# Kernel optimization log

Measured on AMD Instinct MI355X. Metric: run time of the kernel, lower is better.

## Reference

```python
import jax, jax.numpy as jnp
import numpy as np

BN_EPS = 1e-5
K = 9  # 3x3 kernel positions


def conv2d(x, w, b, pad, dil=1):
    out = jax.lax.conv_general_dilated(
        x, w, window_strides=(1, 1), padding=((pad, pad), (pad, pad)),
        rhs_dilation=(dil, dil), dimension_numbers=('NCHW', 'OIHW', 'NCHW'))
    return out + b[None, :, None, None]


def bn_relu(x, g, be, mu, var):
    inv = jax.lax.rsqrt(var + BN_EPS)
    return jax.nn.relu((x - mu[None, :, None, None]) * (g * inv)[None, :, None, None] + be[None, :, None, None])


def deform_conv(x, w_om, b_om, w, b):
    # DCNv2-style modulated deformable 3x3 conv, stride 1, pad 1, dg=1.
    B, C, H, W = x.shape
    om = conv2d(x, w_om, b_om, pad=1)               # [B, 27, H, W]
    o1, o2, m = jnp.split(om, 3, axis=1)            # dy, dx, mask logits: [B,9,H,W]
    mask = jax.nn.sigmoid(m)
    ky, kx = jnp.meshgrid(jnp.arange(3), jnp.arange(3), indexing='ij')
    ky = (ky.reshape(-1) - 1).astype(x.dtype)       # kernel offsets in {-1,0,1}
    kx = (kx.reshape(-1) - 1).astype(x.dtype)
    py = jnp.arange(H, dtype=x.dtype)[None, None, :, None] + ky[None, :, None, None] + o1  # [B,9,H,W]
    px = jnp.arange(W, dtype=x.dtype)[None, None, None, :] + kx[None, :, None, None] + o2

    y0 = jnp.floor(py); x0 = jnp.floor(px)
    wy1 = py - y0; wx1 = px - x0
    y0i = y0.astype(jnp.int32); x0i = x0.astype(jnp.int32)
    x_flat = x.reshape(B, C, H * W)

    def corner(yi, xi, wgt):
        valid = ((yi >= 0) & (yi < H) & (xi >= 0) & (xi < W)).astype(x.dtype)
        idx = jnp.clip(yi, 0, H - 1) * W + jnp.clip(xi, 0, W - 1)      # [B,9,H,W]
        g = jax.vmap(lambda xf, i: xf[:, i])(x_flat, idx.reshape(B, -1))
        g = g.reshape(B, C, K, H, W)
        return g * (wgt * valid)[:, None]

    cols = (corner(y0i,     x0i,     (1 - wy1) * (1 - wx1))
            + corner(y0i,     x0i + 1, (1 - wy1) * wx1)
            + corner(y0i + 1, x0i,     wy1 * (1 - wx1))
            + corner(y0i + 1, x0i + 1, wy1 * wx1))                       # [B,C,9,H,W]
    cols = cols * mask[:, None]
    out = jnp.einsum('bckhw,ock->bohw', cols, w.reshape(w.shape[0], C, K))
    return out + b[None, :, None, None]


def setup_inputs() -> dict:
    key = jax.random.key(0)
    ks = jax.random.split(key, 24)
    B, C, H, W = 2, 64, 256, 256
    d = {}
    d['x'] = jax.random.normal(ks[0], (B, C, H, W), jnp.float32)
    d['w_om'] = jax.random.normal(ks[1], (27, C, 3, 3), jnp.float32) * 0.01
    d['b_om'] = jax.random.normal(ks[2], (27,), jnp.float32) * 0.01
    d['w_dcn'] = jax.random.normal(ks[3], (C, C, 3, 3), jnp.float32) * 0.05
    d['b_dcn'] = jax.random.normal(ks[4], (C,), jnp.float32) * 0.05
    for i, pfx in enumerate(['bn1', 'bn2', 'bn3']):
        d[pfx + '_g'] = jax.random.uniform(ks[5 + 4 * i], (C,), jnp.float32, 0.5, 1.5)
        d[pfx + '_b'] = jax.random.normal(ks[6 + 4 * i], (C,), jnp.float32) * 0.05
        d[pfx + '_m'] = jax.random.normal(ks[7 + 4 * i], (C,), jnp.float32) * 0.05
        d[pfx + '_v'] = jax.random.uniform(ks[8 + 4 * i], (C,), jnp.float32, 0.5, 1.5)
    d['w_h'] = jax.random.normal(ks[17], (C, C, 3, 3), jnp.float32) * 0.05
    d['b_h'] = jax.random.normal(ks[18], (C,), jnp.float32) * 0.05
    d['w_w'] = jax.random.normal(ks[19], (C, C, 3, 3), jnp.float32) * 0.05
    d['b_w'] = jax.random.normal(ks[20], (C,), jnp.float32) * 0.05
    d['w3'] = jax.random.normal(ks[21], (1, C, 3, 3), jnp.float32) * 0.05
    d['b3'] = jax.random.normal(ks[22], (1,), jnp.float32) * 0.05
    return d


def reference(x, w_om, b_om, w_dcn, b_dcn,
              bn1_g, bn1_b, bn1_m, bn1_v,
              w_h, b_h, bn2_g, bn2_b, bn2_m, bn2_v,
              w_w, b_w, bn3_g, bn3_b, bn3_m, bn3_v,
              w3, b3):
    h = deform_conv(x, w_om, b_om, w_dcn, b_dcn)
    h = bn_relu(h, bn1_g, bn1_b, bn1_m, bn1_v)
    h = conv2d(h, w_h, b_h, pad=2, dil=2)
    h = bn_relu(h, bn2_g, bn2_b, bn2_m, bn2_v)
    h = conv2d(h, w_w, b_w, pad=2, dil=2)
    h = bn_relu(h, bn3_g, bn3_b, bn3_m, bn3_v)
    h = conv2d(h, w3, b3, pad=1)
    return jnp.clip(jax.nn.sigmoid(h), 1e-4, 1.0 - 1e-4)
```

## Files before the change

### kernel.cpp

```cpp
#include <hip/hip_runtime.h>
#include <math.h>

#define HH 256
#define WW 256
#define HW (HH*WW)
#define NPX (2*HW)

typedef __attribute__((ext_vector_type(8))) short bf16x8;
typedef __attribute__((ext_vector_type(8))) _Float16 f16x8;
typedef __attribute__((ext_vector_type(2))) _Float16 f16x2;
typedef __attribute__((ext_vector_type(4))) float f32x4;

__device__ __forceinline__ float bf2f(short h) {
    union { unsigned u; float f; } v; v.u = ((unsigned)(unsigned short)h) << 16; return v.f;
}
__device__ __forceinline__ short f2bf(float f) {
    union { float f; unsigned u; } v; v.f = f;
    unsigned r = v.u + 0x7fffu + ((v.u >> 16) & 1u);
    return (short)(r >> 16);
}
__device__ __forceinline__ short f2hs(float f) {
    _Float16 h = (_Float16)f;
    union { _Float16 h; short s; } v; v.h = h; return v.s;
}

__global__ __launch_bounds__(256) void k_x2cl(const float* __restrict__ x,
        short* __restrict__ xcl,
        const float* __restrict__ w_om, const float* __restrict__ w_dcn,
        const float* __restrict__ w_h,  const float* __restrict__ w_w,
        const float* __restrict__ w3,
        short* __restrict__ wt_om, short* __restrict__ wt_dcn,
        short* __restrict__ wt_h,  short* __restrict__ wt_w,
        float* __restrict__ w3t) {
    __shared__ short tile[256 * 66];
    const int xx = threadIdx.x;
    const int row = blockIdx.x;
    const int b = row >> 8, y = row & 255;
    for (int c = 0; c < 64; ++c)
        tile[xx * 66 + c] = f2hs(x[((b * 64 + c) << 16) + (y << 8) + xx]);
    int i = blockIdx.x * 256 + threadIdx.x;
    if (i < 64 * 576) {
        int o = i / 576, k = i - o * 576, t = k >> 6, c = k & 63;
        int kb = k >> 3, j = k & 7;
        int src = (o * 64 + c) * 9 + t;
        int dst = (kb * 64 + o) * 8 + j;
        wt_dcn[dst] = f2hs(w_dcn[src]);
        wt_h[dst]   = f2bf(w_h[src]);
        wt_w[dst]   = f2bf(w_w[src]);
        if (o < 32) wt_om[(kb * 32 + o) * 8 + j] = (o < 27) ? f2hs(w_om[src]) : (short)0;
        if (o == 0) w3t[k] = w3[c * 9 + t];
    }
    __syncthreads();
    short* op = xcl + ((row << 8) + xx) * 64;
#pragma unroll
    for (int j = 0; j < 8; ++j) {
        bf16x8 v;
#pragma unroll
        for (int e = 0; e < 8; ++e) v[e] = tile[xx * 66 + j * 8 + e];
        *(bf16x8*)(op + j * 8) = v;
    }
}

#define XPS 72

__global__ __launch_bounds__(256) __attribute__((amdgpu_waves_per_eu(2, 4)))
void k_dcn_mfma(const short* __restrict__ xcl,
        const short* __restrict__ wom, const float* __restrict__ b_om,
        const short* __restrict__ wt,
        const float* __restrict__ bias,
        const float* __restrict__ gg, const float* __restrict__ be,
        const float* __restrict__ mu, const float* __restrict__ var,
        short* __restrict__ out_cl) {
    __shared__ short xt[256 * XPS];
    __shared__ _Float16 om_lds[64 * 28];
    const int lane = threadIdx.x & 63, wave = threadIdx.x >> 6;
    const int quad = lane >> 4, l16 = lane & 15;
    const int band = blockIdx.x & 7, idx = blockIdx.x >> 3;
    const int tr = band * 8 + (idx >> 5), tc = idx & 31;
    const int b = tr >> 5;
    const int ty0 = (tr & 31) * 8, tx0 = tc * 8;
    const int base = b << 16;
    const int hy0 = ty0 - 4, hx0 = tx0 - 4;
    {
        const int p = threadIdx.x;
        const int sy = min(max(hy0 + (p >> 4), 0), 255);
        const int sx = min(max(hx0 + (p & 15), 0), 255);
        const short* src = xcl + (size_t)((base + sy * 256 + sx) * 64);
        short* dst = &xt[p * XPS];
#pragma unroll
        for (int j = 0; j < 8; ++j)
            *(bf16x8*)(dst + j * 8) = *(const bf16x8*)(src + j * 8);
    }
    __syncthreads();

    const int lp = wave * 16 + l16;
    const int pyy = lp >> 3, pxx = lp & 7;
    const int y = ty0 + pyy, x = tx0 + pxx;

    {
        f32x4 oacc[2];
        oacc[0] = (f32x4){0,0,0,0}; oacc[1] = (f32x4){0,0,0,0};
        auto loadOB = [&](int s, f16x8* Bv) {
            const int kb = s * 4 + quad;
#pragma unroll
            for (int g = 0; g < 2; ++g)
                Bv[g] = *(const f16x8*)(wom + (kb * 32 + g * 16 + l16) * 8);
        };
        f16x8 OB[2][2];
        loadOB(0, OB[0]);
#pragma unroll
        for (int s = 0; s < 18; ++s) {
            if (s < 17) loadOB(s + 1, OB[(s + 1) & 1]);
            const int t = s >> 1, c0 = (s & 1) * 32;
            const int dy = t / 3 - 1, dx = t % 3 - 1;
            f16x8 av = *(const f16x8*)&xt[((pyy + 4 + dy) * 16 + (pxx + 4 + dx)) * XPS + c0 + quad * 8];
            bool ok = ((unsigned)(y + dy) < 256u) && ((unsigned)(x + dx) < 256u);
            if (!ok) { f16x8 z = {0,0,0,0,0,0,0,0}; av = z; }
#pragma unroll
            for (int g = 0; g < 2; ++g)
                oacc[g] = __builtin_amdgcn_mfma_f32_16x16x32_f16(av, OB[s & 1][g], oacc[g], 0, 0, 0);
        }
#pragma unroll
        for (int g = 0; g < 2; ++g) {
            int o = g * 16 + l16;
            if (o < 27) {
                float bo = b_om[o];
#pragma unroll
                for (int r = 0; r < 4; ++r) {
                    float v = oacc[g][r] + bo;
                    if (o >= 18) v = 1.f / (1.f + expf(-v));
                    om_lds[(wave * 16 + quad * 4 + r) * 28 + o] = (_Float16)v;
                }
            }
        }
    }
    __syncthreads();

    f32x4 acc[4];
#pragma unroll
    for (int i = 0; i < 4; ++i) acc[i] = (f32x4){0,0,0,0};

    float omr[27];
#pragma unroll
    for (int j = 0; j < 27; ++j) omr[j] = (float)om_lds[lp * 28 + j];

#pragma unroll
    for (int t = 0; t < 9; ++t) {
        const int ky = t / 3 - 1, kx = t % 3 - 1;
        float o1 = omr[t], o2 = omr[9 + t], m = omr[18 + t];
        float py = (float)(y + ky) + o1;
        float px = (float)(x + kx) + o2;
        float y0f = floorf(py), x0f = floorf(px);
        float wy1 = py - y0f, wx1 = px - x0f;
        int y0 = (int)y0f, xi0 = (int)x0f, y1 = y0 + 1, xi1 = xi0 + 1;
        float w00 = (1.f - wy1) * (1.f - wx1) * m;
        float w01 = (1.f - wy1) * wx1 * m;
        float w10 = wy1 * (1.f - wx1) * m;
        float w11 = wy1 * wx1 * m;
        if (!((unsigned)y0  < 256u)) { w00 = 0.f; w01 = 0.f; }
        if (!((unsigned)y1  < 256u)) { w10 = 0.f; w11 = 0.f; }
        if (!((unsigned)xi0 < 256u)) { w00 = 0.f; w10 = 0.f; }
        if (!((unsigned)xi1 < 256u)) { w01 = 0.f; w11 = 0.f; }
        int cy0 = min(max(y0, 0), 255), cy1 = min(max(y1, 0), 255);
        int cx0 = min(max(xi0, 0), 255), cx1 = min(max(xi1, 0), 255);
        int iy0 = cy0 - hy0, iy1 = cy1 - hy0;
        int ix0 = cx0 - hx0, ix1 = cx1 - hx0;
        bool inh = ((unsigned)iy0 < 16u) && ((unsigned)iy1 < 16u)
                && ((unsigned)ix0 < 16u) && ((unsigned)ix1 < 16u);

        f16x8 C[2][4];
        if (__all(inh)) {
            const int p00 = (iy0 * 16 + ix0) * XPS, p01 = (iy0 * 16 + ix1) * XPS;
            const int p10 = (iy1 * 16 + ix0) * XPS, p11 = (iy1 * 16 + ix1) * XPS;
#pragma unroll
            for (int h = 0; h < 2; ++h) {
                const int cb = h * 32 + quad * 8;
                C[h][0] = *(const f16x8*)&xt[p00 + cb];
                C[h][1] = *(const f16x8*)&xt[p01 + cb];
                C[h][2] = *(const f16x8*)&xt[p10 + cb];
                C[h][3] = *(const f16x8*)&xt[p11 + cb];
            }
        } else {
            const int i00 = (base + cy0 * 256 + cx0) * 64;
            const int i01 = (base + cy0 * 256 + cx1) * 64;
            const int i10 = (base + cy1 * 256 + cx0) * 64;
            const int i11 = (base + cy1 * 256 + cx1) * 64;
#pragma unroll
            for (int h = 0; h < 2; ++h) {
                const int cb = h * 32 + quad * 8;
                C[h][0] = *(const f16x8*)(xcl + i00 + cb);
                C[h][1] = *(const f16x8*)(xcl + i01 + cb);
                C[h][2] = *(const f16x8*)(xcl + i10 + cb);
                C[h][3] = *(const f16x8*)(xcl + i11 + cb);
            }
        }
        const _Float16 h00 = (_Float16)w00, h01 = (_Float16)w01;
        const _Float16 h10 = (_Float16)w10, h11 = (_Float16)w11;
        const f16x2 W00 = {h00, h00}, W01 = {h01, h01};
        const f16x2 W10 = {h10, h10}, W11 = {h11, h11};
#pragma unroll
        for (int h = 0; h < 2; ++h) {
            const f16x2* c0 = (const f16x2*)&C[h][0];
            const f16x2* c1 = (const f16x2*)&C[h][1];
            const f16x2* c2 = (const f16x2*)&C[h][2];
            const f16x2* c3 = (const f16x2*)&C[h][3];
            f16x8 av;
            f16x2* avp = (f16x2*)&av;
#pragma unroll
            for (int d = 0; d < 4; ++d) {
                f16x2 s = c0[d] * W00;
                s = __builtin_elementwise_fma(c1[d], W01, s);
                s = __builtin_elementwise_fma(c2[d], W10, s);
                s = __builtin_elementwise_fma(c3[d], W11, s);
                avp[d] = s;
            }
            const int kb = t * 8 + h * 4 + quad;
#pragma unroll
            for (int g = 0; g < 4; ++g) {
                f16x8 bv = *(const f16x8*)(wt + (kb * 64 + g * 16 + l16) * 8);
                acc[g] = __builtin_amdgcn_mfma_f32_16x16x32_f16(av, bv, acc[g], 0, 0, 0);
            }
        }
    }
#pragma unroll
    for (int g = 0; g < 4; ++g) {
        int o = g * 16 + l16;
        float sc = gg[o] * rsqrtf(var[o] + 1e-5f);
        float off = (bias[o] - mu[o]) * sc + be[o];
#pragma unroll
        for (int r = 0; r < 4; ++r) {
            int mm = quad * 4 + r;
            int pix = base + ((ty0 + wave * 2 + (mm >> 3)) << 8) + tx0 + (mm & 7);
            float v = acc[g][r] * sc + off;
            out_cl[(size_t)pix * 64 + o] = f2bf(fmaxf(v, 0.f));
        }
    }
}

__global__ __launch_bounds__(512) __attribute__((amdgpu_waves_per_eu(2, 4)))
void k_conv_mfma(const short* __restrict__ in_cl,
        const short* __restrict__ wt, const float* __restrict__ bias,
        const float* __restrict__ gg, const float* __restrict__ be,
        const float* __restrict__ mu, const float* __restrict__ var,
        short* __restrict__ out_cl) {
    __shared__ short xt[400 * XPS];
    const int lane = threadIdx.x & 63, wave = threadIdx.x >> 6;
    const int quad = lane >> 4, l16 = lane & 15;
    const int tIdx = (blockIdx.x & 7) * 64 + (blockIdx.x >> 3);
    const int tr = tIdx >> 4, tc = tIdx & 15;
    const int b = tr >> 4;
    const int ty0 = (tr & 15) * 16, tx0 = tc * 16;
    const int base = b << 16;
    if (threadIdx.x < 400) {
        const int p = threadIdx.x;
        const int sy = ty0 - 2 + p / 20, sx = tx0 - 2 + p % 20;
        short* dst = &xt[p * XPS];
        if (((unsigned)sy < 256u) && ((unsigned)sx < 256u)) {
            const short* src = in_cl + (size_t)((base + sy * 256 + sx) * 64);
#pragma unroll
            for (int j = 0; j < 8; ++j)
                *(bf16x8*)(dst + j * 8) = *(const bf16x8*)(src + j * 8);
        } else {
            bf16x8 z = {0,0,0,0,0,0,0,0};
#pragma unroll
            for (int j = 0; j < 8; ++j) *(bf16x8*)(dst + j * 8) = z;
        }
    }
    __syncthreads();
    const int ly = wave * 2;
    f32x4 acc[2][4];
#pragma unroll
    for (int h = 0; h < 2; ++h)
#pragma unroll
        for (int g = 0; g < 4; ++g) acc[h][g] = (f32x4){0,0,0,0};

    auto loadB = [&](int s, bf16x8* Bv) {
        const int kb = s * 4 + quad;
#pragma unroll
        for (int g = 0; g < 4; ++g)
            Bv[g] = *(const bf16x8*)(wt + (kb * 64 + g * 16 + l16) * 8);
    };
    bf16x8 B[3][4];
    loadB(0, B[0]);
    loadB(1, B[1]);
#pragma unroll
    for (int s = 0; s < 18; ++s) {
        if (s + 2 < 18) loadB(s + 2, B[(s + 2) % 3]);
        const int t = s >> 1, c0 = (s & 1) * 32;
        const int dy = (t / 3 - 1) * 2, dx = (t % 3 - 1) * 2;
        const int cidx = c0 + quad * 8;
        bf16x8 a0 = *(const bf16x8*)&xt[((ly + 2 + dy) * 20 + (l16 + 2 + dx)) * XPS + cidx];
        bf16x8 a1 = *(const bf16x8*)&xt[((ly + 3 + dy) * 20 + (l16 + 2 + dx)) * XPS + cidx];
#pragma unroll
        for (int g = 0; g < 4; ++g) {
            acc[0][g] = __builtin_amdgcn_mfma_f32_16x16x32_bf16(a0, B[s % 3][g], acc[0][g], 0, 0, 0);
            acc[1][g] = __builtin_amdgcn_mfma_f32_16x16x32_bf16(a1, B[s % 3][g], acc[1][g], 0, 0, 0);
        }
    }
#pragma unroll
    for (int h = 0; h < 2; ++h)
#pragma unroll
    for (int g = 0; g < 4; ++g) {
        int o = g * 16 + l16;
        float sc = gg[o] * rsqrtf(var[o] + 1e-5f);
        float off = (bias[o] - mu[o]) * sc + be[o];
#pragma unroll
        for (int r = 0; r < 4; ++r) {
            int pix = base + ((ty0 + ly + h) << 8) + tx0 + quad * 4 + r;
            float v = acc[h][g][r] * sc + off;
            out_cl[(size_t)pix * 64 + o] = f2bf(fmaxf(v, 0.f));
        }
    }
}

__global__ __launch_bounds__(256) void k_final(const short* __restrict__ h_cl,
        const float* __restrict__ w3t, const float* __restrict__ b3,
        float* __restrict__ out) {
    __shared__ short xt[324 * XPS];
    const int tIdx = (blockIdx.x & 7) * 64 + (blockIdx.x >> 3);
    const int tr = tIdx >> 4, tc = tIdx & 15;
    const int b = tr >> 4;
    const int ty0 = (tr & 15) * 16, tx0 = tc * 16;
    const int base = b << 16;
    for (int p = threadIdx.x; p < 324; p += 256) {
        const int sy = ty0 - 1 + p / 18, sx = tx0 - 1 + p % 18;
        short* dst = &xt[p * XPS];
        if (((unsigned)sy < 256u) && ((unsigned)sx < 256u)) {
            const short* src = h_cl + (size_t)((base + sy * 256 + sx) * 64);
#pragma unroll
            for (int j = 0; j < 8; ++j)
                *(bf16x8*)(dst + j * 8) = *(const bf16x8*)(src + j * 8);
        } else {
            bf16x8 z = {0,0,0,0,0,0,0,0};
#pragma unroll
            for (int j = 0; j < 8; ++j) *(bf16x8*)(dst + j * 8) = z;
        }
    }
    __syncthreads();
    const int ly = threadIdx.x >> 4, lx = threadIdx.x & 15;
    float acc = 0.f;
#pragma unroll
    for (int t = 0; t < 9; ++t) {
        const int hidx = (ly + 1 + t / 3 - 1) * 18 + (lx + 1 + t % 3 - 1);
        const short* hp = &xt[hidx * XPS];
        const float* wp = w3t + t * 64;
#pragma unroll
        for (int j = 0; j < 64; j += 8) {
            bf16x8 v = *(const bf16x8*)(hp + j);
#pragma unroll
            for (int e = 0; e < 8; ++e)
                acc = fmaf(bf2f(v[e]), wp[j + e], acc);
        }
    }
    float s = 1.f / (1.f + expf(-(acc + b3[0])));
    out[base + ((ty0 + ly) << 8) + tx0 + lx] = fminf(fmaxf(s, 1e-4f), 1.f - 1e-4f);
}

extern "C" void kernel_launch(void* const* d_in, const int* in_sizes, int n_in,
                              void* d_out, int out_size, void* d_ws, size_t ws_size,
                              hipStream_t stream) {
    const float* x     = (const float*)d_in[0];
    const float* w_om  = (const float*)d_in[1];
    const float* b_om  = (const float*)d_in[2];
    const float* w_dcn = (const float*)d_in[3];
    const float* b_dcn = (const float*)d_in[4];
    const float* bn1g = (const float*)d_in[5],  *bn1b = (const float*)d_in[6];
    const float* bn1m = (const float*)d_in[7],  *bn1v = (const float*)d_in[8];
    const float* bn2g = (const float*)d_in[9],  *bn2b = (const float*)d_in[10];
    const float* bn2m = (const float*)d_in[11], *bn2v = (const float*)d_in[12];
    const float* bn3g = (const float*)d_in[13], *bn3b = (const float*)d_in[14];
    const float* bn3m = (const float*)d_in[15], *bn3v = (const float*)d_in[16];
    const float* w_h = (const float*)d_in[17], *b_h = (const float*)d_in[18];
    const float* w_w = (const float*)d_in[19], *b_w = (const float*)d_in[20];
    const float* w3  = (const float*)d_in[21], *b3  = (const float*)d_in[22];
    float* outp = (float*)d_out;

    char* ws = (char*)d_ws;
    short* xcl   = (short*)ws;
    short* h1    = xcl + (size_t)NPX * 64;
    short* h2    = h1 + (size_t)NPX * 64;
    short* wt_om  = h2 + (size_t)NPX * 64;
    short* wt_dcn = wt_om  + 32 * 576;
    short* wt_h   = wt_dcn + 64 * 576;
    short* wt_w   = wt_h   + 64 * 576;
    float* w3t    = (float*)(wt_w + 64 * 576);

    dim3 blk(256);
    k_x2cl<<<512, blk, 0, stream>>>(x, xcl, w_om, w_dcn, w_h, w_w, w3,
                                    wt_om, wt_dcn, wt_h, wt_w, w3t);
    k_dcn_mfma<<<NPX / 64, blk, 0, stream>>>(xcl, wt_om, b_om, wt_dcn, b_dcn,
                                             bn1g, bn1b, bn1m, bn1v, h1);
    k_conv_mfma<<<512, dim3(512), 0, stream>>>(h1, wt_h, b_h, bn2g, bn2b, bn2m, bn2v, h2);
    k_conv_mfma<<<512, dim3(512), 0, stream>>>(h2, wt_w, b_w, bn3g, bn3b, bn3m, bn3v, h1);
    k_final<<<512, blk, 0, stream>>>(h1, w3t, b3, outp);
}
```

Before: 213.0 us.

## Drop LDS halo tile in deformable conv; gather directly from global via cache

Removes the 16x16x64 shared-memory halo tile and its block-wide barrier from the deformable-conv kernel. Both the offset-conv A operands and the bilinear corner samples are now read straight from global memory (relying on L1/L2), and the offset-conv A loads are double-buffered alongside the weight loads. With the LDS use gone, the occupancy hint is raised to 4-8 waves per EU. The aim is to avoid the tile staging cost and the uniform-branch fallback, at the cost of more global/cache traffic and higher latency per gather.

```diff
diff --git a/kernel.cpp b/kernel.cpp
--- a/kernel.cpp
+++ b/kernel.cpp
@@ -63,7 +63,7 @@
 
 #define XPS 72
 
-__global__ __launch_bounds__(256) __attribute__((amdgpu_waves_per_eu(2, 4)))
+__global__ __launch_bounds__(256) __attribute__((amdgpu_waves_per_eu(4, 8)))
 void k_dcn_mfma(const short* __restrict__ xcl,
         const short* __restrict__ wom, const float* __restrict__ b_om,
         const short* __restrict__ wt,
@@ -71,7 +71,6 @@
         const float* __restrict__ gg, const float* __restrict__ be,
         const float* __restrict__ mu, const float* __restrict__ var,
         short* __restrict__ out_cl) {
-    __shared__ short xt[256 * XPS];
     __shared__ _Float16 om_lds[64 * 28];
     const int lane = threadIdx.x & 63, wave = threadIdx.x >> 6;
     const int quad = lane >> 4, l16 = lane & 15;
@@ -80,22 +79,23 @@
     const int b = tr >> 5;
     const int ty0 = (tr & 31) * 8, tx0 = tc * 8;
     const int base = b << 16;
-    const int hy0 = ty0 - 4, hx0 = tx0 - 4;
-    {
-        const int p = threadIdx.x;
-        const int sy = min(max(hy0 + (p >> 4), 0), 255);
-        const int sx = min(max(hx0 + (p & 15), 0), 255);
-        const short* src = xcl + (size_t)((base + sy * 256 + sx) * 64);
-        short* dst = &xt[p * XPS];
-#pragma unroll
-        for (int j = 0; j < 8; ++j)
-            *(bf16x8*)(dst + j * 8) = *(const bf16x8*)(src + j * 8);
-    }
-    __syncthreads();
 
     const int lp = wave * 16 + l16;
     const int pyy = lp >> 3, pxx = lp & 7;
     const int y = ty0 + pyy, x = tx0 + pxx;
+
+    int rb[3], cb3[3];
+#pragma unroll
+    for (int r = 0; r < 3; ++r) {
+        rb[r]  = (base + min(max(y - 1 + r, 0), 255) * 256) * 64;
+        cb3[r] = min(max(x - 1 + r, 0), 255) * 64;
+    }
+    unsigned okm = 0;
+#pragma unroll
+    for (int t = 0; t < 9; ++t) {
+        int dy = t / 3 - 1, dx = t % 3 - 1;
+        if (((unsigned)(y + dy) < 256u) && ((unsigned)(x + dx) < 256u)) okm |= 1u << t;
+    }
 
     {
         f32x4 oacc[2];
@@ -106,16 +106,19 @@
             for (int g = 0; g < 2; ++g)
                 Bv[g] = *(const f16x8*)(wom + (kb * 32 + g * 16 + l16) * 8);
         };
-        f16x8 OB[2][2];
+        auto loadA = [&](int s) -> f16x8 {
+            const int t = s >> 1, c0 = (s & 1) * 32;
+            return *(const f16x8*)(xcl + rb[t / 3] + cb3[t % 3] + c0 + quad * 8);
+        };
+        f16x8 OB[2][2], AV[2];
         loadOB(0, OB[0]);
+        AV[0] = loadA(0);
 #pragma unroll
         for (int s = 0; s < 18; ++s) {
-            if (s < 17) loadOB(s + 1, OB[(s + 1) & 1]);
-            const int t = s >> 1, c0 = (s & 1) * 32;
-            const int dy = t / 3 - 1, dx = t % 3 - 1;
-            f16x8 av = *(const f16x8*)&xt[((pyy + 4 + dy) * 16 + (pxx + 4 + dx)) * XPS + c0 + quad * 8];
-            bool ok = ((unsigned)(y + dy) < 256u) && ((unsigned)(x + dx) < 256u);
-            if (!ok) { f16x8 z = {0,0,0,0,0,0,0,0}; av = z; }
+            if (s < 17) { loadOB(s + 1, OB[(s + 1) & 1]); AV[(s + 1) & 1] = loadA(s + 1); }
+            const int t = s >> 1;
+            f16x8 av = AV[s & 1];
+            if (!((okm >> t) & 1u)) { f16x8 z = {0,0,0,0,0,0,0,0}; av = z; }
 #pragma unroll
             for (int g = 0; g < 2; ++g)
                 oacc[g] = __builtin_amdgcn_mfma_f32_16x16x32_f16(av, OB[s & 1][g], oacc[g], 0, 0, 0);
@@ -163,36 +166,18 @@
         if (!((unsigned)xi1 < 256u)) { w01 = 0.f; w11 = 0.f; }
         int cy0 = min(max(y0, 0), 255), cy1 = min(max(y1, 0), 255);
         int cx0 = min(max(xi0, 0), 255), cx1 = min(max(xi1, 0), 255);
-        int iy0 = cy0 - hy0, iy1 = cy1 - hy0;
-        int ix0 = cx0 - hx0, ix1 = cx1 - hx0;
-        bool inh = ((unsigned)iy0 < 16u) && ((unsigned)iy1 < 16u)
-                && ((unsigned)ix0 < 16u) && ((unsigned)ix1 < 16u);
+        const int ry0 = (base + cy0 * 256) * 64, ry1 = (base + cy1 * 256) * 64;
+        const int i00 = ry0 + cx0 * 64, i01 = ry0 + cx1 * 64;
+        const int i10 = ry1 + cx0 * 64, i11 = ry1 + cx1 * 64;
 
         f16x8 C[2][4];
-        if (__all(inh)) {
-            const int p00 = (iy0 * 16 + ix0) * XPS, p01 = (iy0 * 16 + ix1) * XPS;
-            const int p10 = (iy1 * 16 + ix0) * XPS, p11 = (iy1 * 16 + ix1) * XPS;
-#pragma unroll
-            for (int h = 0; h < 2; ++h) {
-                const int cb = h * 32 + quad * 8;
-                C[h][0] = *(const f16x8*)&xt[p00 + cb];
-                C[h][1] = *(const f16x8*)&xt[p01 + cb];
-                C[h][2] = *(const f16x8*)&xt[p10 + cb];
-                C[h][3] = *(const f16x8*)&xt[p11 + cb];
-            }
-        } else {
-            const int i00 = (base + cy0 * 256 + cx0) * 64;
-            const int i01 = (base + cy0 * 256 + cx1) * 64;
-            const int i10 = (base + cy1 * 256 + cx0) * 64;
-            const int i11 = (base + cy1 * 256 + cx1) * 64;
-#pragma unroll
-            for (int h = 0; h < 2; ++h) {
-                const int cb = h * 32 + quad * 8;
-                C[h][0] = *(const f16x8*)(xcl + i00 + cb);
-                C[h][1] = *(const f16x8*)(xcl + i01 + cb);
-                C[h][2] = *(const f16x8*)(xcl + i10 + cb);
-                C[h][3] = *(const f16x8*)(xcl + i11 + cb);
-            }
+#pragma unroll
+        for (int h = 0; h < 2; ++h) {
+            const int cb = h * 32 + quad * 8;
+            C[h][0] = *(const f16x8*)(xcl + i00 + cb);
+            C[h][1] = *(const f16x8*)(xcl + i01 + cb);
+            C[h][2] = *(const f16x8*)(xcl + i10 + cb);
+            C[h][3] = *(const f16x8*)(xcl + i11 + cb);
         }
         const _Float16 h00 = (_Float16)w00, h01 = (_Float16)w01;
         const _Float16 h10 = (_Float16)w10, h11 = (_Float16)w11;
```

Result: slower. 276.1 us (+29.6%).
